# Optimization experiments

Measured on AMD Instinct MI355X. Metric: run time of the kernel, lower is better.

The kernel has to match this reference:

```python
import jax, jax.numpy as jnp
import numpy as np

B, L, D_MODEL, HEAD = 8, 2048, 1024, 64

def setup_inputs() -> dict:
    key = jax.random.key(0)
    ks = jax.random.split(key, 6)
    idx_k = jax.random.normal(ks[0], (B, L, D_MODEL), dtype=jnp.float32)
    idx_q = jax.random.normal(ks[1], (B, L, D_MODEL), dtype=jnp.float32)
    idx_v = jax.random.normal(ks[2], (B, L, D_MODEL), dtype=jnp.float32)
    # causal lower-triangular mask, broadcast over batch
    msk = jnp.tril(jnp.ones((L, L), dtype=jnp.int32))
    s = 1.0 / np.sqrt(D_MODEL)
    Wk = jax.random.uniform(ks[3], (D_MODEL, HEAD), jnp.float32, -s, s)
    Wq = jax.random.uniform(ks[4], (D_MODEL, HEAD), jnp.float32, -s, s)
    Wv = jax.random.uniform(ks[5], (D_MODEL, HEAD), jnp.float32, -s, s)
    return {"idx_k": idx_k, "idx_q": idx_q, "idx_v": idx_v, "msk": msk,
            "Wk": Wk, "Wq": Wq, "Wv": Wv}

def reference(idx_k, idx_q, idx_v, msk, Wk, Wq, Wv):
    # projections (Linear, no bias): [B,L,d_model] @ [d_model,head] -> [B,L,head]
    K = idx_k @ Wk
    Q = idx_q @ Wq
    V = idx_v @ Wv
    scale = K.shape[-1] ** -0.5
    # scores: [B,Lq,Lk]
    S = jnp.einsum('bqh,bkh->bqk', Q, K) * scale
    S = jnp.where(msk == 0, jnp.float32(-1e9), S)
    att = jax.nn.softmax(S, axis=-1)  # dropout=0.0 (inference)
    out = jnp.einsum('bqk,bkh->bqh', att, V)
    return out
```

## Files before the change

### kernel.cpp

```cpp
#include <hip/hip_runtime.h>

typedef __bf16 bf16x8 __attribute__((ext_vector_type(8)));
typedef float f32x4 __attribute__((ext_vector_type(4)));
typedef unsigned short u16;

#define LSEQ 2048
#define DMODEL 1024
#define HEADD 64
#define NBATCH 8

__device__ __forceinline__ u16 cvt(float f) {
  __bf16 h = (__bf16)f;
  return __builtin_bit_cast(u16, h);
}

#define BARRIER_LGKM() do {                                   \
    asm volatile("s_waitcnt lgkmcnt(0)" ::: "memory");        \
    __builtin_amdgcn_sched_barrier(0);                        \
    __builtin_amdgcn_s_barrier();                             \
    __builtin_amdgcn_sched_barrier(0);                        \
  } while (0)

__global__ __launch_bounds__(256) void wt_kernel(
    const float* __restrict__ Wk, const float* __restrict__ Wq,
    const float* __restrict__ Wv, u16* __restrict__ wp) {
  int idx = blockIdx.x * 256 + threadIdx.x;
  int j = idx & 7;
  int lane = (idx >> 3) & 63;
  int ks = (idx >> 9) & 31;
  int c = (idx >> 14) & 3;
  int p = idx >> 16;
  const float* W = (p == 0) ? Wk : ((p == 1) ? Wq : Wv);
  int k = ks * 32 + 8 * (lane >> 4) + j;
  int col = 16 * c + (lane & 15);
  wp[idx] = cvt(W[(size_t)k * HEADD + col]);
}

__global__ __launch_bounds__(128) void proj_kernel(
    const float* __restrict__ ik, const float* __restrict__ iq, const float* __restrict__ iv,
    const u16* __restrict__ wp, u16* __restrict__ Kb, u16* __restrict__ Qb,
    u16* __restrict__ Vt) {
  __shared__ __align__(16) u16 Asw[2][32 * 128];
  int p = blockIdx.y;
  const float* A = (p == 0) ? ik : ((p == 1) ? iq : iv);
  const u16* Wp = wp + (size_t)p * 4 * 32 * 512;
  int t = threadIdx.x;
  int lane = t & 63;
  int wv = t >> 6;
  int l15 = lane & 15, g = lane >> 4;
  int rowbase = blockIdx.x * 32;
  const float* srcbase = A + (size_t)rowbase * DMODEL;

  int srow0 = t >> 5;
  int scol = (t & 31) * 4;

  float4 stgA[8], stgB[8];
  bf16x8 wfr[4][4];

  auto issue = [&](float4 (&stg)[8], int kc) {
#pragma unroll
    for (int i = 0; i < 8; ++i)
      stg[i] = *(const float4*)(srcbase + (size_t)(i * 4 + srow0) * DMODEL + kc + scol);
  };
  auto commit = [&](const float4 (&stg)[8], u16* basep) {
    char* base = (char*)basep;
#pragma unroll
    for (int i = 0; i < 8; ++i) {
      int row = i * 4 + srow0;
      ushort4 pk;
      pk.x = cvt(stg[i].x); pk.y = cvt(stg[i].y);
      pk.z = cvt(stg[i].z); pk.w = cvt(stg[i].w);
      int byte = row * 256 + ((scol * 2) ^ ((row & 7) << 4));
      *(ushort4*)(base + byte) = pk;
    }
  };
  auto wload = [&](int c8) {
#pragma unroll
    for (int ks = 0; ks < 4; ++ks)
#pragma unroll
      for (int c = 0; c < 4; ++c)
        wfr[ks][c] = *(const bf16x8*)(Wp + ((size_t)c * 32 + c8 * 4 + ks) * 512 + lane * 8);
  };

  f32x4 acc[4] = {};
  int abase = (16 * wv + l15) * 256;
  int aswz = (l15 & 7) << 4;

  auto computeC = [&](const char* lbase) {
#pragma unroll
    for (int ks = 0; ks < 4; ++ks) {
      bf16x8 af = *(const bf16x8*)(lbase + abase + ((ks * 64 + 16 * g) ^ aswz));
#pragma unroll
      for (int c = 0; c < 4; ++c)
        acc[c] = __builtin_amdgcn_mfma_f32_16x16x32_bf16(af, wfr[ks][c], acc[c], 0, 0, 0);
    }
  };

  issue(stgA, 0);
  issue(stgB, 128);
  commit(stgA, &Asw[0][0]);
  BARRIER_LGKM();

#pragma unroll 1
  for (int cc = 0; cc < 8; cc += 2) {
    wload(cc);
    __builtin_amdgcn_sched_barrier(0);
    if (cc < 6) issue(stgA, (cc + 2) * 128);
    __builtin_amdgcn_sched_barrier(0);
    computeC((const char*)&Asw[0][0]);
    commit(stgB, &Asw[1][0]);
    BARRIER_LGKM();
    wload(cc + 1);
    __builtin_amdgcn_sched_barrier(0);
    if (cc < 5) issue(stgB, (cc + 3) * 128);
    __builtin_amdgcn_sched_barrier(0);
    computeC((const char*)&Asw[1][0]);
    if (cc < 6) commit(stgA, &Asw[0][0]);
    BARRIER_LGKM();
  }

  int rb2 = rowbase + 16 * wv;
  if (p == 2) {
    int row0 = rb2 + 4 * g;
    int b = row0 >> 11, tok = row0 & 2047;
#pragma unroll
    for (int c = 0; c < 4; ++c) {
      int d = 16 * c + l15;
      ushort4 pk;
      pk.x = cvt(acc[c][0]); pk.y = cvt(acc[c][1]);
      pk.z = cvt(acc[c][2]); pk.w = cvt(acc[c][3]);
      *(ushort4*)(Vt + ((size_t)b * HEADD + d) * LSEQ + tok) = pk;
    }
  } else {
    u16* dst = (p == 0) ? Kb : Qb;
    float s = (p == 1) ? 0.125f : 1.0f;
#pragma unroll
    for (int c = 0; c < 4; ++c)
#pragma unroll
      for (int r = 0; r < 4; ++r)
        dst[(size_t)(rb2 + 4 * g + r) * HEADD + 16 * c + l15] = cvt(acc[c][r] * s);
  }
}

__global__ __launch_bounds__(128) void attn_kernel(
    const u16* __restrict__ Kb, const u16* __restrict__ Qb, const u16* __restrict__ Vt,
    float* __restrict__ out) {
  __shared__ __align__(16) u16 plds[2][16 * 40];
  __shared__ __align__(16) float mrg[64][18];
  int lane = threadIdx.x & 63;
  int wv = threadIdx.x >> 6;
  int l15 = lane & 15, g = lane >> 4;
  int id = blockIdx.x;
  int b = id & 7;
  int qt = 127 - (id >> 3);
  int qbase = qt * 16;

  const u16* Qp = Qb + ((size_t)b * LSEQ + qbase) * HEADD;
  const u16* Kp = Kb + (size_t)b * LSEQ * HEADD;
  const u16* Vp = Vt + (size_t)b * HEADD * LSEQ;

  bf16x8 qf[2];
#pragma unroll
  for (int ds = 0; ds < 2; ++ds)
    qf[ds] = *(const bf16x8*)(Qp + (size_t)l15 * HEADD + 32 * ds + 8 * g);

  f32x4 acc[4] = {};
  float m = -1e30f, lsum = 0.f;
  int q_abs = qbase + l15;
  int ntiles = (qbase + 47) >> 5;

  for (int t = wv; t < ntiles; t += 2) {
    int kbase = t * 32;
    f32x4 sacc[2] = {};
#pragma unroll
    for (int f = 0; f < 2; ++f)
#pragma unroll
      for (int ds = 0; ds < 2; ++ds) {
        bf16x8 kf = *(const bf16x8*)(Kp + (size_t)(kbase + 16 * f + l15) * HEADD + 32 * ds + 8 * g);
        sacc[f] = __builtin_amdgcn_mfma_f32_16x16x32_bf16(kf, qf[ds], sacc[f], 0, 0, 0);
      }

    float sv[2][4];
    float tmax = -1e30f;
#pragma unroll
    for (int f = 0; f < 2; ++f)
#pragma unroll
      for (int r = 0; r < 4; ++r) {
        int key = kbase + 16 * f + 4 * g + r;
        float s = (key <= q_abs) ? sacc[f][r] : -1e30f;
        sv[f][r] = s;
        tmax = fmaxf(tmax, s);
      }
    tmax = fmaxf(tmax, __shfl_xor(tmax, 16));
    tmax = fmaxf(tmax, __shfl_xor(tmax, 32));
    float mnew = fmaxf(m, tmax);
    float al = __expf(m - mnew);
    float pv[2][4];
    float rs = 0.f;
#pragma unroll
    for (int f = 0; f < 2; ++f)
#pragma unroll
      for (int r = 0; r < 4; ++r) {
        pv[f][r] = __expf(sv[f][r] - mnew);
        rs += pv[f][r];
      }
    rs += __shfl_xor(rs, 16);
    rs += __shfl_xor(rs, 32);
    lsum = lsum * al + rs;
    m = mnew;

    float alr[4];
#pragma unroll
    for (int r = 0; r < 4; ++r) alr[r] = __shfl(al, 4 * g + r);
#pragma unroll
    for (int c = 0; c < 4; ++c)
#pragma unroll
      for (int r = 0; r < 4; ++r) acc[c][r] *= alr[r];

#pragma unroll
    for (int f = 0; f < 2; ++f) {
      ushort4 pk;
      pk.x = cvt(pv[f][0]); pk.y = cvt(pv[f][1]);
      pk.z = cvt(pv[f][2]); pk.w = cvt(pv[f][3]);
      *(ushort4*)&plds[wv][l15 * 40 + 16 * f + 4 * g] = pk;
    }
    bf16x8 ap = *(const bf16x8*)&plds[wv][l15 * 40 + 8 * g];

#pragma unroll
    for (int c = 0; c < 4; ++c) {
      bf16x8 vf = *(const bf16x8*)(Vp + (size_t)(16 * c + l15) * LSEQ + kbase + 8 * g);
      acc[c] = __builtin_amdgcn_mfma_f32_16x16x32_bf16(ap, vf, acc[c], 0, 0, 0);
    }
  }

  if (wv == 1) {
#pragma unroll
    for (int c = 0; c < 4; ++c)
#pragma unroll
      for (int r = 0; r < 4; ++r) mrg[lane][c * 4 + r] = acc[c][r];
    mrg[lane][16] = m;
    mrg[lane][17] = lsum;
  }
  __syncthreads();
  if (wv == 0) {
    float m1 = mrg[lane][16], l1 = mrg[lane][17];
    float mT = fmaxf(m, m1);
    float e0 = __expf(m - mT), e1 = __expf(m1 - mT);
    float lT = lsum * e0 + l1 * e1;
    float e0r[4], e1r[4], li[4];
#pragma unroll
    for (int r = 0; r < 4; ++r) {
      e0r[r] = __shfl(e0, 4 * g + r);
      e1r[r] = __shfl(e1, 4 * g + r);
      li[r] = 1.0f / __shfl(lT, 4 * g + r);
    }
#pragma unroll
    for (int c = 0; c < 4; ++c)
#pragma unroll
      for (int r = 0; r < 4; ++r) {
        float v = acc[c][r] * e0r[r] + mrg[lane][c * 4 + r] * e1r[r];
        out[((size_t)b * LSEQ + qbase + 4 * g + r) * HEADD + 16 * c + l15] = v * li[r];
      }
  }
}

extern "C" void kernel_launch(void* const* d_in, const int* in_sizes, int n_in,
                              void* d_out, int out_size, void* d_ws, size_t ws_size,
                              hipStream_t stream) {
  const float* idx_k = (const float*)d_in[0];
  const float* idx_q = (const float*)d_in[1];
  const float* idx_v = (const float*)d_in[2];
  const float* Wk = (const float*)d_in[4];
  const float* Wq = (const float*)d_in[5];
  const float* Wv = (const float*)d_in[6];
  float* out = (float*)d_out;

  char* ws = (char*)d_ws;
  const size_t WT_BYTES = (size_t)3 * 4 * 32 * 512 * 2;
  const size_t MAT_BYTES = (size_t)NBATCH * LSEQ * HEADD * 2;
  u16* wp = (u16*)ws;
  u16* Kb = (u16*)(ws + WT_BYTES);
  u16* Qb = (u16*)(ws + WT_BYTES + MAT_BYTES);
  u16* Vt = (u16*)(ws + WT_BYTES + 2 * MAT_BYTES);

  hipLaunchKernelGGL(wt_kernel, dim3(768), dim3(256), 0, stream, Wk, Wq, Wv, wp);
  hipLaunchKernelGGL(proj_kernel, dim3(512, 3), dim3(128), 0, stream,
                     idx_k, idx_q, idx_v, wp, Kb, Qb, Vt);
  hipLaunchKernelGGL(attn_kernel, dim3(1024), dim3(128), 0, stream, Kb, Qb, Vt, out);
}
```

Baseline: 82.05 us.

## Halve projection row tile and split output columns across the two waves

```diff
diff --git a/kernel.cpp b/kernel.cpp
--- a/kernel.cpp
+++ b/kernel.cpp
@@ -40,7 +40,7 @@
     const float* __restrict__ ik, const float* __restrict__ iq, const float* __restrict__ iv,
     const u16* __restrict__ wp, u16* __restrict__ Kb, u16* __restrict__ Qb,
     u16* __restrict__ Vt) {
-  __shared__ __align__(16) u16 Asw[2][32 * 128];
+  __shared__ __align__(16) u16 Asw[2][16 * 128];
   int p = blockIdx.y;
   const float* A = (p == 0) ? ik : ((p == 1) ? iq : iv);
   const u16* Wp = wp + (size_t)p * 4 * 32 * 512;
@@ -48,24 +48,24 @@
   int lane = t & 63;
   int wv = t >> 6;
   int l15 = lane & 15, g = lane >> 4;
-  int rowbase = blockIdx.x * 32;
+  int rowbase = blockIdx.x * 16;
   const float* srcbase = A + (size_t)rowbase * DMODEL;
 
   int srow0 = t >> 5;
   int scol = (t & 31) * 4;
 
-  float4 stgA[8], stgB[8];
-  bf16x8 wfr[4][4];
-
-  auto issue = [&](float4 (&stg)[8], int kc) {
-#pragma unroll
-    for (int i = 0; i < 8; ++i)
+  float4 stgA[4], stgB[4];
+  bf16x8 wfr[4][2];
+
+  auto issue = [&](float4 (&stg)[4], int kc) {
+#pragma unroll
+    for (int i = 0; i < 4; ++i)
       stg[i] = *(const float4*)(srcbase + (size_t)(i * 4 + srow0) * DMODEL + kc + scol);
   };
-  auto commit = [&](const float4 (&stg)[8], u16* basep) {
+  auto commit = [&](const float4 (&stg)[4], u16* basep) {
     char* base = (char*)basep;
 #pragma unroll
-    for (int i = 0; i < 8; ++i) {
+    for (int i = 0; i < 4; ++i) {
       int row = i * 4 + srow0;
       ushort4 pk;
       pk.x = cvt(stg[i].x); pk.y = cvt(stg[i].y);
@@ -78,12 +78,13 @@
 #pragma unroll
     for (int ks = 0; ks < 4; ++ks)
 #pragma unroll
-      for (int c = 0; c < 4; ++c)
-        wfr[ks][c] = *(const bf16x8*)(Wp + ((size_t)c * 32 + c8 * 4 + ks) * 512 + lane * 8);
-  };
-
-  f32x4 acc[4] = {};
-  int abase = (16 * wv + l15) * 256;
+      for (int cc = 0; cc < 2; ++cc)
+        wfr[ks][cc] = *(const bf16x8*)(
+            Wp + ((size_t)(wv * 2 + cc) * 32 + c8 * 4 + ks) * 512 + lane * 8);
+  };
+
+  f32x4 acc[2] = {};
+  int abase = l15 * 256;
   int aswz = (l15 & 7) << 4;
 
   auto computeC = [&](const char* lbase) {
@@ -91,8 +92,8 @@
     for (int ks = 0; ks < 4; ++ks) {
       bf16x8 af = *(const bf16x8*)(lbase + abase + ((ks * 64 + 16 * g) ^ aswz));
 #pragma unroll
-      for (int c = 0; c < 4; ++c)
-        acc[c] = __builtin_amdgcn_mfma_f32_16x16x32_bf16(af, wfr[ks][c], acc[c], 0, 0, 0);
+      for (int cc = 0; cc < 2; ++cc)
+        acc[cc] = __builtin_amdgcn_mfma_f32_16x16x32_bf16(af, wfr[ks][cc], acc[cc], 0, 0, 0);
     }
   };
 
@@ -102,43 +103,43 @@
   BARRIER_LGKM();
 
 #pragma unroll 1
-  for (int cc = 0; cc < 8; cc += 2) {
-    wload(cc);
-    __builtin_amdgcn_sched_barrier(0);
-    if (cc < 6) issue(stgA, (cc + 2) * 128);
+  for (int cc8 = 0; cc8 < 8; cc8 += 2) {
+    wload(cc8);
+    __builtin_amdgcn_sched_barrier(0);
+    if (cc8 < 6) issue(stgA, (cc8 + 2) * 128);
     __builtin_amdgcn_sched_barrier(0);
     computeC((const char*)&Asw[0][0]);
     commit(stgB, &Asw[1][0]);
     BARRIER_LGKM();
-    wload(cc + 1);
-    __builtin_amdgcn_sched_barrier(0);
-    if (cc < 5) issue(stgB, (cc + 3) * 128);
+    wload(cc8 + 1);
+    __builtin_amdgcn_sched_barrier(0);
+    if (cc8 < 5) issue(stgB, (cc8 + 3) * 128);
     __builtin_amdgcn_sched_barrier(0);
     computeC((const char*)&Asw[1][0]);
-    if (cc < 6) commit(stgA, &Asw[0][0]);
+    if (cc8 < 6) commit(stgA, &Asw[0][0]);
     BARRIER_LGKM();
   }
 
-  int rb2 = rowbase + 16 * wv;
   if (p == 2) {
-    int row0 = rb2 + 4 * g;
+    int row0 = rowbase + 4 * g;
     int b = row0 >> 11, tok = row0 & 2047;
 #pragma unroll
-    for (int c = 0; c < 4; ++c) {
-      int d = 16 * c + l15;
+    for (int cc = 0; cc < 2; ++cc) {
+      int d = 16 * (wv * 2 + cc) + l15;
       ushort4 pk;
-      pk.x = cvt(acc[c][0]); pk.y = cvt(acc[c][1]);
-      pk.z = cvt(acc[c][2]); pk.w = cvt(acc[c][3]);
+      pk.x = cvt(acc[cc][0]); pk.y = cvt(acc[cc][1]);
+      pk.z = cvt(acc[cc][2]); pk.w = cvt(acc[cc][3]);
       *(ushort4*)(Vt + ((size_t)b * HEADD + d) * LSEQ + tok) = pk;
     }
   } else {
     u16* dst = (p == 0) ? Kb : Qb;
     float s = (p == 1) ? 0.125f : 1.0f;
 #pragma unroll
-    for (int c = 0; c < 4; ++c)
+    for (int cc = 0; cc < 2; ++cc)
 #pragma unroll
       for (int r = 0; r < 4; ++r)
-        dst[(size_t)(rb2 + 4 * g + r) * HEADD + 16 * c + l15] = cvt(acc[c][r] * s);
+        dst[(size_t)(rowbase + 4 * g + r) * HEADD + 16 * (wv * 2 + cc) + l15] =
+            cvt(acc[cc][r] * s);
   }
 }
 
@@ -284,7 +285,7 @@
   u16* Vt = (u16*)(ws + WT_BYTES + 2 * MAT_BYTES);
 
   hipLaunchKernelGGL(wt_kernel, dim3(768), dim3(256), 0, stream, Wk, Wq, Wv, wp);
-  hipLaunchKernelGGL(proj_kernel, dim3(512, 3), dim3(128), 0, stream,
+  hipLaunchKernelGGL(proj_kernel, dim3(1024, 3), dim3(128), 0, stream,
                      idx_k, idx_q, idx_v, wp, Kb, Qb, Vt);
   hipLaunchKernelGGL(attn_kernel, dim3(1024), dim3(128), 0, stream, Kb, Qb, Vt, out);
 }
```

Result: slower. 86.25 us (+5.1%).
